# Kernel tuning notes

Measured on AMD Instinct MI355X. Metric: run time of the kernel, lower is better.

The kernel has to match this reference:

```python
import jax, jax.numpy as jnp
import numpy as np
from jax import lax

N_C = 1024  # number of FPS centroids (hard-coded in forward)
K = 32      # knn neighbors (hard-coded in forward)


def _fps(x, far0):
    # Faithful to the source: dist is recomputed against ONLY the latest
    # centroid each iteration (the mask/min-update in the source is dead code),
    # then far = argmax(dist).
    B = x.shape[0]
    bidx = jnp.arange(B)

    def step(far, _):
        c = x[bidx, far]                              # [B, C]
        d = jnp.sum((x - c[:, None, :]) ** 2, -1)     # [B, N]
        return jnp.argmax(d, -1), c

    _, cents = lax.scan(step, far0, None, length=N_C)  # cents: [n_c, B, C]
    return jnp.transpose(cents, (1, 0, 2))             # [B, n_c, C]


def _knn_group(x, cent):
    # squared euclidean distances (same argsort order as torch.cdist)
    d2 = (jnp.sum(cent ** 2, -1)[..., None]
          + jnp.sum(x ** 2, -1)[:, None, :]
          - 2.0 * jnp.einsum('bmc,bnc->bmn', cent, x))   # [B, n_c, N]
    _, idx = lax.top_k(-d2, K)                            # [B, n_c, K] smallest dists
    neighbors = jax.vmap(lambda xb, ib: xb[ib])(x, idx)   # [B, n_c, K, C]
    return neighbors


def _conv1x1(h, w, b):
    # 1x1 Conv1d == channel matmul; h: [B, Cin, L], w: [Cout, Cin]
    return jax.nn.relu(jnp.einsum('oi,bil->bol', w, h) + b[None, :, None])


def setup_inputs() -> dict:
    key = jax.random.key(0)
    ks = jax.random.split(key, 20)
    B, N, C = 4, 16384, 3
    num_classes = 3
    p = lambda k, shp: (jax.random.normal(k, shp, jnp.float32) * 0.02)
    return {
        'x': jax.random.normal(ks[0], (B, N, C), jnp.float32),
        'far_init': jax.random.randint(ks[1], (B,), 0, N, jnp.int32),
        'w1': p(ks[2], (64, 3)),    'b1': p(ks[3], (64,)),
        'w2': p(ks[4], (64, 64)),   'b2': p(ks[5], (64,)),
        'w3': p(ks[6], (64, 64)),   'b3': p(ks[7], (64,)),
        'w4': p(ks[8], (128, 64)),  'b4': p(ks[9], (128,)),
        'w5': p(ks[10], (1024, 128)), 'b5': p(ks[11], (1024,)),
        'fw1': p(ks[12], (512, 1024)), 'fb1': p(ks[13], (512,)),
        'fw2': p(ks[14], (256, 512)),  'fb2': p(ks[15], (256,)),
        'fw3': p(ks[16], (num_classes, 256)), 'fb3': p(ks[17], (num_classes,)),
    }


def reference(x, far_init, w1, b1, w2, b2, w3, b3, w4, b4, w5, b5,
              fw1, fb1, fw2, fb2, fw3, fb3):
    B, N, C = x.shape
    cent = _fps(x, far_init)                 # [B, n_c, C]
    neighbors = _knn_group(x, cent)          # [B, n_c, K, C]
    h = jnp.transpose(neighbors, (0, 3, 1, 2)).reshape(B, C, N_C * K)
    h = _conv1x1(h, w1, b1)
    h = _conv1x1(h, w2, b2)
    h = _conv1x1(h, w3, b3)
    h = _conv1x1(h, w4, b4)
    h = _conv1x1(h, w5, b5)                  # [B, 1024, n_c*K]
    g = jnp.max(h, axis=2)                   # global max pool -> [B, 1024]
    g = jax.nn.relu(g @ fw1.T + fb1)
    g = jax.nn.relu(g @ fw2.T + fb2)
    return g @ fw3.T + fb3                   # [B, num_classes]
```

## Files before the change

kernel.cpp:

```cpp
#include <hip/hip_runtime.h>

#define BN  4
#define NPT 16384
#define NCC 1024
#define KNN 32

#define HBINS    2048
#define CCH      2
#define CAND_CAP 768

#define NBLK 64

#define OFF_CCOUNT 0
#define OFF_SCOUNT 64
#define OFF_SBITS  128
#define OFF_POOL   (128 + BN*(NPT/32)*4)
#define OFF_CLIST  (OFF_POOL + BN*NCC*4)
#define OFF_H1     (OFF_CLIST + BN*NCC*4)
#define OFF_H2     (OFF_H1 + BN*512*4)
#define OFF_SLIST  (OFF_H2 + BN*256*4)
#define OFF_BAR    (OFF_SLIST + BN*NPT*4)

typedef short bf16x8 __attribute__((ext_vector_type(8)));
typedef float f32x4  __attribute__((ext_vector_type(4)));
typedef float f32x2  __attribute__((ext_vector_type(2)));

__device__ __forceinline__ short f2bf(float f) {
    unsigned u = __float_as_uint(f);
    return (short)((u + 0x7fffu + ((u >> 16) & 1u)) >> 16);
}
__device__ __forceinline__ bf16x8 cvt8(const float* __restrict__ p) {
    bf16x8 v;
#pragma unroll
    for (int j = 0; j < 8; ++j) v[j] = f2bf(p[j]);
    return v;
}

template <typename T>
__device__ __forceinline__ void ast(T* p, T v) {
    __hip_atomic_store(p, v, __ATOMIC_RELAXED, __HIP_MEMORY_SCOPE_AGENT);
}
template <typename T>
__device__ __forceinline__ T ald(const T* p) {
    return __hip_atomic_load(const_cast<T*>(p), __ATOMIC_RELAXED, __HIP_MEMORY_SCOPE_AGENT);
}

__device__ __forceinline__ void gridbar(unsigned* __restrict__ bar, int ph) {
    __syncthreads();
    if (threadIdx.x == 0) {
        __hip_atomic_fetch_add(&bar[ph], 1u, __ATOMIC_RELAXED, __HIP_MEMORY_SCOPE_AGENT);
        while (__hip_atomic_load(&bar[ph], __ATOMIC_RELAXED, __HIP_MEMORY_SCOPE_AGENT)
               < (unsigned)NBLK)
            __builtin_amdgcn_s_sleep(8);
    }
    __syncthreads();
}

__device__ __forceinline__ unsigned key_of(float px, float py, float pz, float xn,
                                           float cx, float cy, float cz, float cn)
{
    float dot = __fadd_rn(__fadd_rn(__fmul_rn(cx,px), __fmul_rn(cy,py)), __fmul_rn(cz,pz));
    float d2  = __fsub_rn(__fadd_rn(cn, xn), __fmul_rn(2.0f, dot));
    unsigned u = __float_as_uint(d2);
    return u ^ ((u >> 31) ? 0xFFFFFFFFu : 0x80000000u);
}

__device__ __forceinline__ void wave_scan_bins(const unsigned* __restrict__ H,
    int nbins, int rem, int lane, int* __restrict__ out_bin, int* __restrict__ out_below)
{
    int per = nbins >> 6;
    int base = lane * per;
    unsigned part = 0;
    for (int q = 0; q < per; ++q) part += H[base + q];
    unsigned inc = part;
#pragma unroll
    for (int m = 1; m < 64; m <<= 1) {
        unsigned u = __shfl_up(inc, m, 64);
        if (lane >= m) inc += u;
    }
    unsigned exc = inc - part;
    unsigned long long mk = __ballot(exc < (unsigned)rem && inc >= (unsigned)rem);
    int src = __ffsll((long long)mk) - 1;
    if (lane == src) {
        unsigned run = exc; int bb = base;
        for (int q = 0; q < per; ++q) {
            unsigned h = H[base + q];
            if (run + h >= (unsigned)rem) { bb = base + q; break; }
            run += h;
        }
        *out_bin = bb; *out_below = (int)run;
    }
}

#define MFMA16(a, bfr, c) __builtin_amdgcn_mfma_f32_16x16x32_bf16(a, bfr, c, 0, 0, 0)

__global__ __launch_bounds__(1024) void mega_kernel(const float* __restrict__ x,
    const int* __restrict__ far_init,
    const float* __restrict__ w1, const float* __restrict__ b1,
    const float* __restrict__ w2, const float* __restrict__ b2,
    const float* __restrict__ w3, const float* __restrict__ b3,
    const float* __restrict__ w4, const float* __restrict__ b4,
    const float* __restrict__ w5, const float* __restrict__ b5,
    const float* __restrict__ fw1, const float* __restrict__ fb1,
    const float* __restrict__ fw2, const float* __restrict__ fb2,
    const float* __restrict__ fw3, const float* __restrict__ fb3,
    int* __restrict__ clist, int* __restrict__ ccount, int* __restrict__ scount,
    unsigned* __restrict__ sbits, int* __restrict__ slist, float* __restrict__ pool,
    float* __restrict__ h1g, float* __restrict__ h2g, float* __restrict__ out,
    unsigned* __restrict__ bar)
{
    const int blk = blockIdx.x, t = threadIdx.x;
    __shared__ __align__(16) char smem[36864];

    {
#pragma clang fp contract(off)
        if (blk < 4) {
            const int b = blk;
            unsigned char* seen = (unsigned char*)smem;
            unsigned long long* slot = (unsigned long long*)(smem + 16384);

            if (t < 512) ast(&sbits[b*(NPT/32) + t], 0u);
            ast(&pool[b*NCC + t], 0.0f);
            if (t == 0) { ast(&ccount[b], 0); ast(&scount[b], 0); }

            const float* xb = x + (size_t)b * NPT * 3;
            f32x2 px[8], py[8], pz[8];
#pragma unroll
            for (int r = 0; r < 8; ++r) {
                int ia = t + ((2*r) << 10), ib = ia + 1024;
                px[r] = f32x2{xb[ia*3+0], xb[ib*3+0]};
                py[r] = f32x2{xb[ia*3+1], xb[ib*3+1]};
                pz[r] = f32x2{xb[ia*3+2], xb[ib*3+2]};
            }
            ((uint4*)seen)[t] = make_uint4(0,0,0,0);
            if (t == 0) { slot[0] = 0ull; slot[1] = 0ull; slot[2] = 0ull; }
            int prev_bx = far_init[b];
            __syncthreads();
            int pbs = __builtin_amdgcn_readfirstlane(prev_bx);
            float cx = xb[pbs*3], cy = xb[pbs*3+1], cz = xb[pbs*3+2];

            int done = 0;
            for (int it = 0; it < NCC-1; ++it) {
                const int p = it % 3;
                const f32x2 cX = {cx, cx}, cY = {cy, cy}, cZ = {cz, cz};
                float best = -1.0f; int bi = 0;
#pragma unroll
                for (int r = 0; r < 8; ++r) {
                    f32x2 dx = px[r] - cX;
                    f32x2 dy = py[r] - cY;
                    f32x2 dz = pz[r] - cZ;
                    f32x2 m1 = dx * dx;
                    f32x2 m2 = dy * dy;
                    f32x2 m3 = dz * dz;
                    f32x2 s  = (m1 + m2) + m3;
                    int ia = t + ((2*r) << 10);
                    if (s.x > best) { best = s.x; bi = ia; }
                    if (s.y > best) { best = s.y; bi = ia + 1024; }
                }
#pragma unroll
                for (int m = 1; m < 64; m <<= 1) {
                    float od = __shfl_xor(best, m, 64);
                    int   oi = __shfl_xor(bi,   m, 64);
                    if (od > best || (od == best && oi < bi)) { best = od; bi = oi; }
                }
                if ((t & 63) == 0) {
                    unsigned long long pk =
                        (((unsigned long long)__float_as_uint(best)) << 32)
                        | (unsigned)(NPT - 1 - bi);
                    atomicMax(&slot[p], pk);
                }
                if (t == 0) seen[prev_bx] = 1;
                __syncthreads();
                int bx = NPT - 1 - (int)(unsigned)(slot[p] & 0xFFFFFFFFull);
                if (t == 0) slot[(it + 2) % 3] = 0ull;
                if (seen[bx]) { done = 1; break; }
                prev_bx = bx;
                int bxs = __builtin_amdgcn_readfirstlane(bx);
                cx = xb[bxs*3]; cy = xb[bxs*3+1]; cz = xb[bxs*3+2];
            }
            if (!done && t == 0) seen[prev_bx] = 1;
            __syncthreads();
#pragma unroll
            for (int j = 0; j < 16; ++j) {
                int idx = t + (j << 10);
                if (seen[idx]) {
                    int pos = atomicAdd(&ccount[b], 1);
                    ast(&clist[b * NCC + pos], idx);
                }
            }
        }
    }
    gridbar(bar, 0);

    {
        const int c0 = ald(&ccount[0]), c1 = ald(&ccount[1]);
        const int c2 = ald(&ccount[2]), c3 = ald(&ccount[3]);
        const int maxc = max(max(c0,c1), max(c2,c3));
        unsigned* hist    = (unsigned*)smem;
        unsigned* cand    = (unsigned*)(smem + 16384);
        float*    cpx     = (float*)(smem + 22528);
        float*    cpy     = cpx + CCH;
        float*    cpz     = cpy + CCH;
        float*    cpn     = cpz + CCH;
        unsigned* candCnt = (unsigned*)(cpn + CCH);
        int*      s_bb    = (int*)(candCnt + CCH);
        int*      s_below = s_bb + CCH;
        int*      s_rrem  = s_below + CCH;
        int*      s_need  = s_rrem + CCH;
        int*      s_pref  = s_need + CCH;
        unsigned* s_tau   = (unsigned*)(s_pref + CCH);
        int*      s_tb    = (int*)(s_tau + CCH);

        const int lane = t & 63, w = t >> 6;

        for (int wi = blk; (wi >> 2) * CCH < maxc; wi += NBLK) {
            const int b = wi & 3;
            const int cnt = (b==0) ? c0 : (b==1) ? c1 : (b==2) ? c2 : c3;
            const int cbase = (wi >> 2) * CCH;
            if (cbase >= cnt) continue;
            const float* xb = x + (size_t)b * NPT * 3;

            __syncthreads();
            if (t < CCH) {
                int ci = ald(&clist[b * NCC + min(cbase + t, cnt - 1)]);
                float cx = xb[ci*3], cy = xb[ci*3+1], cz = xb[ci*3+2];
                cpx[t] = cx; cpy[t] = cy; cpz[t] = cz;
                cpn[t] = __fadd_rn(__fadd_rn(__fmul_rn(cx,cx), __fmul_rn(cy,cy)), __fmul_rn(cz,cz));
                candCnt[t] = 0;
            }
            for (int i = t; i < CCH * HBINS; i += 1024) hist[i] = 0;
            __syncthreads();

            unsigned keys[NPT/1024][CCH];
#pragma unroll
            for (int j = 0; j < NPT/1024; ++j) {
                int i = t + (j << 10);
                float px = xb[i*3], py = xb[i*3+1], pz = xb[i*3+2];
                float xn = __fadd_rn(__fadd_rn(__fmul_rn(px,px), __fmul_rn(py,py)), __fmul_rn(pz,pz));
#pragma unroll
                for (int c = 0; c < CCH; ++c) {
                    unsigned key = key_of(px,py,pz,xn, cpx[c],cpy[c],cpz[c],cpn[c]);
                    keys[j][c] = key;
                    atomicAdd(&hist[c*HBINS + (key >> 21)], 1u);
                }
            }
            __syncthreads();

            if (w < CCH)
                wave_scan_bins(&hist[w*HBINS], HBINS, KNN, lane, &s_bb[w], &s_below[w]);
            __syncthreads();
            if (t < CCH) s_rrem[t] = KNN - s_below[t];
            __syncthreads();

#pragma unroll
            for (int j = 0; j < NPT/1024; ++j) {
#pragma unroll
                for (int c = 0; c < CCH; ++c) {
                    unsigned key = keys[j][c];
                    if ((int)(key >> 21) == s_bb[c]) {
                        unsigned pos = atomicAdd(&candCnt[c], 1u);
                        if (pos < CAND_CAP) cand[c*CAND_CAP + pos] = key;
                    }
                }
            }
            __syncthreads();

            if (w < CCH) {
                unsigned cc = candCnt[w];
                if (cc <= CAND_CAP) {
                    int r = s_rrem[w] - 1;
                    const unsigned* C = &cand[w*CAND_CAP];
                    for (int idx = lane; idx < (int)cc; idx += 64) {
                        unsigned k = C[idx]; int rank = 0;
                        for (int q = 0; q < (int)cc; ++q) {
                            unsigned kq = C[q];
                            rank += (kq < k || (kq == k && q < idx)) ? 1 : 0;
                        }
                        if (rank == r) s_tau[w] = k;
                    }
                    if (lane == 0) s_need[w] = 0;
                } else if (lane == 0) s_need[w] = 1;
            }
            __syncthreads();

            for (int c = 0; c < CCH; ++c) {
                if (s_need[c]) {
                    const float cx = cpx[c], cy = cpy[c], cz = cpz[c], cn = cpn[c];
                    for (int i = t; i < HBINS; i += 1024) hist[i] = 0;
                    __syncthreads();
                    for (int j = 0; j < NPT/1024; ++j) {
                        int i = t + (j << 10);
                        float px = xb[i*3], py = xb[i*3+1], pz = xb[i*3+2];
                        float xn = __fadd_rn(__fadd_rn(__fmul_rn(px,px), __fmul_rn(py,py)), __fmul_rn(pz,pz));
                        unsigned key = key_of(px,py,pz,xn, cx,cy,cz,cn);
                        if ((int)(key >> 21) == s_bb[c]) atomicAdd(&hist[(key >> 10) & 2047u], 1u);
                    }
                    __syncthreads();
                    if (w == 0) wave_scan_bins(hist, HBINS, s_rrem[c], lane, &s_tb[0], &s_tb[1]);
                    __syncthreads();
                    if (t == 0) { s_pref[c] = (s_bb[c] << 11) | s_tb[0]; s_rrem[c] -= s_tb[1]; }
                    __syncthreads();
                    for (int i = t; i < 1024; i += 1024) hist[i] = 0;
                    __syncthreads();
                    for (int j = 0; j < NPT/1024; ++j) {
                        int i = t + (j << 10);
                        float px = xb[i*3], py = xb[i*3+1], pz = xb[i*3+2];
                        float xn = __fadd_rn(__fadd_rn(__fmul_rn(px,px), __fmul_rn(py,py)), __fmul_rn(pz,pz));
                        unsigned key = key_of(px,py,pz,xn, cx,cy,cz,cn);
                        if ((int)(key >> 10) == s_pref[c]) atomicAdd(&hist[key & 1023u], 1u);
                    }
                    __syncthreads();
                    if (w == 0) wave_scan_bins(hist, 1024, s_rrem[c], lane, &s_tb[0], &s_tb[1]);
                    __syncthreads();
                    if (t == 0) s_tau[c] = (((unsigned)s_pref[c]) << 10) | (unsigned)s_tb[0];
                    __syncthreads();
                }
            }
            __syncthreads();

#pragma unroll
            for (int j = 0; j < NPT/1024; ++j) {
                int i = t + (j << 10);
                bool sel = false;
#pragma unroll
                for (int c = 0; c < CCH; ++c) sel |= (keys[j][c] <= s_tau[c]);
                if (sel) {
                    unsigned bit = 1u << (i & 31);
                    unsigned old = atomicOr(&sbits[b*(NPT/32) + (i >> 5)], bit);
                    if (!(old & bit)) {
                        int pos = atomicAdd(&scount[b], 1);
                        ast(&slist[b * NPT + pos], i);
                    }
                }
            }
        }
    }
    gridbar(bar, 1);

    {
        const int s0 = ald(&scount[0]), s1 = ald(&scount[1]);
        const int s2 = ald(&scount[2]), s3 = ald(&scount[3]);
        short* A1 = (short*)smem;
        short* A2 = (short*)(smem + 9216);
        short* A3 = (short*)(smem + 18432);
        float* sx = (float*)(smem + 35840);

        const int lane = t & 63;
        const int w    = __builtin_amdgcn_readfirstlane(t >> 6);
        const int m    = lane & 15, quad = lane >> 4;
        const int b    = blk & 3;
        const int z    = (blk >> 2) & 3;
        const int cnt  = (b==0) ? s0 : (b==1) ? s1 : (b==2) ? s2 : s3;

        const int ocA = (w >> 2) * 16 + m;
        bf16x8 bw2[2], bw3[2], bw4[2][2], bw5[4];
#pragma unroll
        for (int ks = 0; ks < 2; ++ks) {
            bw2[ks] = cvt8(w2 + ocA*64 + ks*32 + quad*8);
            bw3[ks] = cvt8(w3 + ocA*64 + ks*32 + quad*8);
        }
        int oc4i[2];
#pragma unroll
        for (int r2 = 0; r2 < 2; ++r2) {
            oc4i[r2] = ((w >> 2) + 4*r2) * 16 + m;
#pragma unroll
            for (int ks = 0; ks < 2; ++ks)
                bw4[r2][ks] = cvt8(w4 + oc4i[r2]*64 + ks*32 + quad*8);
        }
        const int oc5 = z*256 + w*16 + m;
#pragma unroll
        for (int ks = 0; ks < 4; ++ks)
            bw5[ks] = cvt8(w5 + oc5*128 + ks*32 + quad*8);
        const float bias2 = b2[ocA], bias3 = b3[ocA];
        const float bias4_0 = b4[oc4i[0]], bias4_1 = b4[oc4i[1]];
        const float bias5 = b5[oc5];
        float w1v[4][3], b1v[4];
#pragma unroll
        for (int i = 0; i < 4; ++i) {
            int oc = w*4 + i;
            w1v[i][0] = w1[oc*3+0]; w1v[i][1] = w1[oc*3+1]; w1v[i][2] = w1[oc*3+2];
            b1v[i] = b1[oc];
        }
        const int pt0 = (w & 3) * 16;

        for (int xblk = blk >> 4; xblk * 64 < cnt; xblk += 4) {
            const int base = xblk << 6;
            const int npts = min(64, cnt - base);
            __syncthreads();
            if (t < 64) {
                int idx = ald(&slist[b * NPT + base + min(t, npts - 1)]);
                const float* xp = x + ((size_t)b * NPT + idx) * 3;
                sx[t] = xp[0]; sx[64 + t] = xp[1]; sx[128 + t] = xp[2];
            }
            __syncthreads();
            {
                float x0 = sx[lane], x1 = sx[64 + lane], x2 = sx[128 + lane];
#pragma unroll
                for (int i = 0; i < 4; ++i) {
                    float acc = fmaf(x2, w1v[i][2], fmaf(x1, w1v[i][1],
                                 fmaf(x0, w1v[i][0], b1v[i])));
                    A1[lane*72 + w*4 + i] = f2bf(fmaxf(acc, 0.0f));
                }
            }
            __syncthreads();
            {
                bf16x8 a0 = *(const bf16x8*)&A1[(pt0 + m)*72 + quad*8];
                bf16x8 a1 = *(const bf16x8*)&A1[(pt0 + m)*72 + 32 + quad*8];
                f32x4 d = {0.f, 0.f, 0.f, 0.f};
                d = MFMA16(a0, bw2[0], d);
                d = MFMA16(a1, bw2[1], d);
#pragma unroll
                for (int r = 0; r < 4; ++r)
                    A2[(pt0 + quad*4 + r)*72 + ocA] = f2bf(fmaxf(d[r] + bias2, 0.0f));
            }
            __syncthreads();
            {
                bf16x8 a0 = *(const bf16x8*)&A2[(pt0 + m)*72 + quad*8];
                bf16x8 a1 = *(const bf16x8*)&A2[(pt0 + m)*72 + 32 + quad*8];
                f32x4 d = {0.f, 0.f, 0.f, 0.f};
                d = MFMA16(a0, bw3[0], d);
                d = MFMA16(a1, bw3[1], d);
#pragma unroll
                for (int r = 0; r < 4; ++r)
                    A1[(pt0 + quad*4 + r)*72 + ocA] = f2bf(fmaxf(d[r] + bias3, 0.0f));
            }
            __syncthreads();
            {
                bf16x8 a0 = *(const bf16x8*)&A1[(pt0 + m)*72 + quad*8];
                bf16x8 a1 = *(const bf16x8*)&A1[(pt0 + m)*72 + 32 + quad*8];
#pragma unroll
                for (int r2 = 0; r2 < 2; ++r2) {
                    f32x4 d = {0.f, 0.f, 0.f, 0.f};
                    d = MFMA16(a0, bw4[r2][0], d);
                    d = MFMA16(a1, bw4[r2][1], d);
                    float bs = r2 ? bias4_1 : bias4_0;
#pragma unroll
                    for (int r = 0; r < 4; ++r)
                        A3[(pt0 + quad*4 + r)*136 + oc4i[r2]] = f2bf(fmaxf(d[r] + bs, 0.0f));
                }
            }
            __syncthreads();
            {
                float vm = 0.0f;
#pragma unroll
                for (int pt4 = 0; pt4 < 4; ++pt4) {
                    const int q0 = pt4 * 16;
                    f32x4 d = {0.f, 0.f, 0.f, 0.f};
#pragma unroll
                    for (int ks = 0; ks < 4; ++ks) {
                        bf16x8 a = *(const bf16x8*)&A3[(q0 + m)*136 + ks*32 + quad*8];
                        d = MFMA16(a, bw5[ks], d);
                    }
#pragma unroll
                    for (int r = 0; r < 4; ++r)
                        vm = fmaxf(vm, fmaxf(d[r] + bias5, 0.0f));
                }
                vm = fmaxf(vm, __shfl_xor(vm, 16, 64));
                vm = fmaxf(vm, __shfl_xor(vm, 32, 64));
                if (lane < 16)
                    atomicMax((int*)&pool[b*NCC + z*256 + w*16 + lane], __float_as_int(vm));
            }
        }
    }
    gridbar(bar, 2);

    {
        const int bo = blk >> 2, b = blk & 3;
        const int lane = t & 63, w = t >> 6;
        float* g = (float*)smem;
        g[t] = ald(&pool[b*NCC + t]);
        __syncthreads();
#pragma unroll
        for (int i = 0; i < 2; ++i) {
            int o = bo * 32 + w * 2 + i;
            float acc = 0.0f;
#pragma unroll
            for (int j = 0; j < 16; ++j) {
                int k = lane + (j << 6);
                acc += g[k] * fw1[o*1024 + k];
            }
#pragma unroll
            for (int m = 1; m < 64; m <<= 1) acc += __shfl_xor(acc, m, 64);
            if (lane == 0) ast(&h1g[b*512 + o], fmaxf(acc + fb1[o], 0.0f));
        }
    }
    gridbar(bar, 3);

    if (blk < 32) {
        const int bo = blk >> 2, b = blk & 3;
        const int lane = t & 63, w = t >> 6;
        float* h1 = (float*)smem;
        if (t < 512) h1[t] = ald(&h1g[b*512 + t]);
        __syncthreads();
#pragma unroll
        for (int i = 0; i < 2; ++i) {
            int o = bo * 32 + w * 2 + i;
            float acc = 0.0f;
#pragma unroll
            for (int j = 0; j < 8; ++j) {
                int k = lane + (j << 6);
                acc += h1[k] * fw2[o*512 + k];
            }
#pragma unroll
            for (int m = 1; m < 64; m <<= 1) acc += __shfl_xor(acc, m, 64);
            if (lane == 0) ast(&h2g[b*256 + o], fmaxf(acc + fb2[o], 0.0f));
        }
    }
    gridbar(bar, 4);

    if (blk < 4) {
        const int b = blk;
        const int lane = t & 63, w = t >> 6;
        float* h2 = (float*)smem;
        if (t < 256) h2[t] = ald(&h2g[b*256 + t]);
        __syncthreads();
        if (t < 256 && w < 3) {
            float acc = 0.0f;
#pragma unroll
            for (int j = 0; j < 4; ++j) {
                int k = lane + (j << 6);
                acc += h2[k] * fw3[w*256 + k];
            }
#pragma unroll
            for (int m = 1; m < 64; m <<= 1) acc += __shfl_xor(acc, m, 64);
            if (lane == 0) out[b*3 + w] = acc + fb3[w];
        }
    }
}

extern "C" void kernel_launch(void* const* d_in, const int* in_sizes, int n_in,
                              void* d_out, int out_size, void* d_ws, size_t ws_size,
                              hipStream_t stream)
{
    const float* x    = (const float*)d_in[0];
    const int*   far0 = (const int*)  d_in[1];
    const float *w1 = (const float*)d_in[2],  *b1 = (const float*)d_in[3];
    const float *w2 = (const float*)d_in[4],  *b2 = (const float*)d_in[5];
    const float *w3 = (const float*)d_in[6],  *b3 = (const float*)d_in[7];
    const float *w4 = (const float*)d_in[8],  *b4 = (const float*)d_in[9];
    const float *w5 = (const float*)d_in[10], *b5 = (const float*)d_in[11];
    const float *fw1 = (const float*)d_in[12], *fb1 = (const float*)d_in[13];
    const float *fw2 = (const float*)d_in[14], *fb2 = (const float*)d_in[15];
    const float *fw3 = (const float*)d_in[16], *fb3 = (const float*)d_in[17];

    char* ws = (char*)d_ws;
    int*      ccount = (int*)     (ws + OFF_CCOUNT);
    int*      scount = (int*)     (ws + OFF_SCOUNT);
    unsigned* sbits  = (unsigned*)(ws + OFF_SBITS);
    float*    pool   = (float*)   (ws + OFF_POOL);
    int*      clist  = (int*)     (ws + OFF_CLIST);
    float*    h1g    = (float*)   (ws + OFF_H1);
    float*    h2g    = (float*)   (ws + OFF_H2);
    int*      slist  = (int*)     (ws + OFF_SLIST);
    unsigned* bar    = (unsigned*)(ws + OFF_BAR);

    (void)hipMemsetAsync(bar, 0, 8 * sizeof(unsigned), stream);
    mega_kernel<<<NBLK, 1024, 0, stream>>>(x, far0,
        w1,b1, w2,b2, w3,b3, w4,b4, w5,b5, fw1,fb1, fw2,fb2, fw3,fb3,
        clist, ccount, scount, sbits, slist, pool, h1g, h2g, (float*)d_out, bar);
}
```

Measured before the change: 158.0 us.

## Split FPS argmax into float max plus index pass, prefetch weights on idle blocks

The FPS loop's per-wave packed 64-bit argmax shuffle is replaced by a cheaper float-only max reduction. A second pass finds the lowest matching index and shares its coordinates through LDS, which avoids the dependent global reload of the centroid in most cases. Meanwhile the 60 blocks that sit idle during FPS stream the MLP and FC weights so they are warm in cache for later phases, and the grid barrier polls more often. The cost is an extra __syncthreads per FPS iteration plus extra memory traffic while FPS runs.

```diff
diff --git a/kernel.cpp b/kernel.cpp
--- a/kernel.cpp
+++ b/kernel.cpp
@@ -51,9 +51,20 @@
         __hip_atomic_fetch_add(&bar[ph], 1u, __ATOMIC_RELAXED, __HIP_MEMORY_SCOPE_AGENT);
         while (__hip_atomic_load(&bar[ph], __ATOMIC_RELAXED, __HIP_MEMORY_SCOPE_AGENT)
                < (unsigned)NBLK)
-            __builtin_amdgcn_s_sleep(8);
+            __builtin_amdgcn_s_sleep(2);
     }
     __syncthreads();
+}
+
+__device__ __forceinline__ float pf4(const float* __restrict__ p, int nfloat,
+                                     int t, float acc) {
+    const float4* q = (const float4*)p;
+    const int n4 = nfloat >> 2;
+    for (int i = t; i < n4; i += 1024) {
+        float4 v = q[i];
+        acc += (v.x + v.y) + (v.z + v.w);
+    }
+    return acc;
 }
 
 __device__ __forceinline__ unsigned key_of(float px, float py, float pz, float xn,
@@ -116,8 +127,11 @@
 #pragma clang fp contract(off)
         if (blk < 4) {
             const int b = blk;
-            unsigned char* seen = (unsigned char*)smem;
-            unsigned long long* slot = (unsigned long long*)(smem + 16384);
+            unsigned char* seen   = (unsigned char*)smem;
+            unsigned*      vslot  = (unsigned*)(smem + 16384);
+            int*           islot  = (int*)(smem + 16384 + 8);
+            int*           nmatch = (int*)(smem + 16384 + 16);
+            int4*          cslot  = (int4*)(smem + 16384 + 32);
 
             if (t < 512) ast(&sbits[b*(NPT/32) + t], 0u);
             ast(&pool[b*NCC + t], 0.0f);
@@ -133,7 +147,11 @@
                 pz[r] = f32x2{xb[ia*3+2], xb[ib*3+2]};
             }
             ((uint4*)seen)[t] = make_uint4(0,0,0,0);
-            if (t == 0) { slot[0] = 0ull; slot[1] = 0ull; slot[2] = 0ull; }
+            if (t == 0) {
+                vslot[0] = 0u;         vslot[1] = 0u;
+                islot[0] = 0x7fffffff; islot[1] = 0x7fffffff;
+                nmatch[0] = 0;         nmatch[1] = 0;
+            }
             int prev_bx = far_init[b];
             __syncthreads();
             int pbs = __builtin_amdgcn_readfirstlane(prev_bx);
@@ -141,9 +159,10 @@
 
             int done = 0;
             for (int it = 0; it < NCC-1; ++it) {
-                const int p = it % 3;
+                const int p = it & 1;
                 const f32x2 cX = {cx, cx}, cY = {cy, cy}, cZ = {cz, cz};
-                float best = -1.0f; int bi = 0;
+                f32x2 sv[8];
+                f32x2 rm = {0.0f, 0.0f};
 #pragma unroll
                 for (int r = 0; r < 8; ++r) {
                     f32x2 dx = px[r] - cX;
@@ -153,30 +172,62 @@
                     f32x2 m2 = dy * dy;
                     f32x2 m3 = dz * dz;
                     f32x2 s  = (m1 + m2) + m3;
-                    int ia = t + ((2*r) << 10);
-                    if (s.x > best) { best = s.x; bi = ia; }
-                    if (s.y > best) { best = s.y; bi = ia + 1024; }
-                }
-#pragma unroll
-                for (int m = 1; m < 64; m <<= 1) {
-                    float od = __shfl_xor(best, m, 64);
-                    int   oi = __shfl_xor(bi,   m, 64);
-                    if (od > best || (od == best && oi < bi)) { best = od; bi = oi; }
-                }
-                if ((t & 63) == 0) {
-                    unsigned long long pk =
-                        (((unsigned long long)__float_as_uint(best)) << 32)
-                        | (unsigned)(NPT - 1 - bi);
-                    atomicMax(&slot[p], pk);
-                }
+                    sv[r] = s;
+                    rm.x = fmaxf(rm.x, s.x);
+                    rm.y = fmaxf(rm.y, s.y);
+                }
+                float tm = fmaxf(rm.x, rm.y);
+#pragma unroll
+                for (int m = 1; m < 64; m <<= 1)
+                    tm = fmaxf(tm, __shfl_xor(tm, m, 64));
+                if ((t & 63) == 0) atomicMax(&vslot[p], __float_as_uint(tm));
                 if (t == 0) seen[prev_bx] = 1;
                 __syncthreads();
-                int bx = NPT - 1 - (int)(unsigned)(slot[p] & 0xFFFFFFFFull);
-                if (t == 0) slot[(it + 2) % 3] = 0ull;
+                const unsigned bmax = vslot[p];
+                if (t == 0) {
+                    vslot[p^1] = 0u; islot[p^1] = 0x7fffffff; nmatch[p^1] = 0;
+                }
+                if (__float_as_uint(tm) == bmax) {
+                    int   myidx = 0x7fffffff;
+                    float mx = 0.f, my = 0.f, mz = 0.f;
+#pragma unroll
+                    for (int r = 0; r < 8; ++r) {
+                        int ia = t + ((2*r) << 10);
+                        if (__float_as_uint(sv[r].x) == bmax && ia < myidx)
+                            { myidx = ia;        mx = px[r].x; my = py[r].x; mz = pz[r].x; }
+                        if (__float_as_uint(sv[r].y) == bmax && ia + 1024 < myidx)
+                            { myidx = ia + 1024; mx = px[r].y; my = py[r].y; mz = pz[r].y; }
+                    }
+                    if (myidx != 0x7fffffff) {
+                        atomicMin(&islot[p], myidx);
+                        int cs = atomicAdd(&nmatch[p], 1);
+                        if (cs < 4)
+                            cslot[p*4 + cs] = make_int4(myidx, __float_as_int(mx),
+                                                        __float_as_int(my), __float_as_int(mz));
+                    }
+                }
+                __syncthreads();
+                const int bx = islot[p];
                 if (seen[bx]) { done = 1; break; }
                 prev_bx = bx;
-                int bxs = __builtin_amdgcn_readfirstlane(bx);
-                cx = xb[bxs*3]; cy = xb[bxs*3+1]; cz = xb[bxs*3+2];
+                const int nm = nmatch[p] < 4 ? nmatch[p] : 4;
+                bool got = false;
+                float nx = 0.f, ny = 0.f, nz = 0.f;
+#pragma unroll
+                for (int csi = 0; csi < 4; ++csi) {
+                    if (csi < nm) {
+                        int4 v = cslot[p*4 + csi];
+                        if (v.x == bx) {
+                            nx = __int_as_float(v.y); ny = __int_as_float(v.z);
+                            nz = __int_as_float(v.w); got = true;
+                        }
+                    }
+                }
+                if (got) { cx = nx; cy = ny; cz = nz; }
+                else {
+                    int bxs = __builtin_amdgcn_readfirstlane(bx);
+                    cx = xb[bxs*3]; cy = xb[bxs*3+1]; cz = xb[bxs*3+2];
+                }
             }
             if (!done && t == 0) seen[prev_bx] = 1;
             __syncthreads();
@@ -188,6 +239,22 @@
                     ast(&clist[b * NCC + pos], idx);
                 }
             }
+        } else {
+            float acc = 0.0f;
+            const int bo = blk >> 2;
+            acc = pf4(fw1 + bo*32*1024, 32*1024, t, acc);
+            if (blk < 32) acc = pf4(fw2 + bo*32*512, 32*512, t, acc);
+            acc = pf4(w5 + (bo & 3)*256*128, 256*128, t, acc);
+            if (blk < 12) {
+                acc = pf4(w2, 64*64, t, acc);
+                acc = pf4(w3, 64*64, t, acc);
+                acc = pf4(w4, 128*64, t, acc);
+            }
+            if (blk < 8) {
+                acc = pf4(fw1, 32*1024, t, acc);
+                acc = pf4(fw2, 32*512, t, acc);
+            }
+            asm volatile("" :: "v"(acc));
         }
     }
     gridbar(bar, 0);
```

New measurement: 166.9 us. +5.7%, slower.
